# Performance work log

Hardware: AMD Instinct MI355X
Metric: run time of the kernel (lower is better)

## Reference

```python
import jax, jax.numpy as jnp
import numpy as np

NUM_PHONES = 39
BLANK = NUM_PHONES  # blank appended as last class
NEG = -1e30  # finite stand-in for -inf (log-space)


def ctc_loss(lp, targets, input_lengths, target_lengths, blank):
    """lp: (T, B, C) log-probs. Returns torch-style CTCLoss(reduction='mean', zero_infinity=True)."""
    T, B, C = lp.shape
    L = targets.shape[1]
    S = 2 * L + 1
    # extended label sequence: blank, l1, blank, l2, ..., blank
    ext = jnp.full((B, S), blank, dtype=targets.dtype).at[:, 1::2].set(targets)
    ext_m2 = jnp.concatenate([jnp.full((B, 2), blank, dtype=ext.dtype), ext[:, :-2]], axis=1)
    skip = (ext != blank) & (ext != ext_m2)  # (B, S) allow s-2 transition
    # per-step emission log-probs gathered at extended labels: (T, B, S)
    emit = jnp.take_along_axis(lp, jnp.broadcast_to(ext[None], (T, B, S)), axis=2)

    alpha0 = jnp.full((B, S), NEG, dtype=lp.dtype)
    alpha0 = alpha0.at[:, 0].set(emit[0, :, 0]).at[:, 1].set(emit[0, :, 1])
    pad1 = jnp.full((B, 1), NEG, dtype=lp.dtype)
    pad2 = jnp.full((B, 2), NEG, dtype=lp.dtype)

    def step(alpha, xs):
        emit_t, t = xs
        a1 = jnp.concatenate([pad1, alpha[:, :-1]], axis=1)
        a2 = jnp.where(skip, jnp.concatenate([pad2, alpha[:, :-2]], axis=1), NEG)
        m = jnp.maximum(jnp.maximum(alpha, a1), a2)
        new = m + jnp.log(jnp.exp(alpha - m) + jnp.exp(a1 - m) + jnp.exp(a2 - m)) + emit_t
        new = jnp.where((t < input_lengths)[:, None], new, alpha)  # freeze past length
        return new, None

    alpha, _ = jax.lax.scan(step, alpha0, (emit[1:], jnp.arange(1, T)))
    end = 2 * target_lengths  # index of final blank in extended sequence
    a_blank = jnp.take_along_axis(alpha, end[:, None], axis=1)[:, 0]
    a_label = jnp.take_along_axis(alpha, (end - 1)[:, None], axis=1)[:, 0]
    loss_b = -jnp.logaddexp(a_blank, a_label)
    loss_b = jnp.where(loss_b > 1e29, 0.0, loss_b)  # zero_infinity
    return jnp.mean(loss_b / target_lengths.astype(lp.dtype))


def setup_inputs() -> dict:
    B, T, H, L = 32, 2000, 512, 200
    C = NUM_PHONES + 1
    key = jax.random.key(0)
    k1, k2, k3 = jax.random.split(key, 3)
    hidden = jax.random.normal(k1, (B, T, H), dtype=jnp.float32)
    W = jax.random.normal(k2, (C, H), dtype=jnp.float32) / np.sqrt(H)
    b = jnp.zeros((C,), dtype=jnp.float32)
    targets = jax.random.randint(k3, (B, L), 0, NUM_PHONES, dtype=jnp.int32)
    input_lengths = jnp.full((B,), T, dtype=jnp.int32)
    target_lengths = jnp.full((B,), L, dtype=jnp.int32)
    return {"hidden": hidden, "W": W, "b": b, "targets": targets,
            "input_lengths": input_lengths, "target_lengths": target_lengths}


def reference(hidden, W, b, targets, input_lengths, target_lengths):
    # dropout is identity in eval mode
    logits = jnp.einsum('bth,ch->btc', hidden, W) + b
    log_prob = jax.nn.log_softmax(logits, axis=-1).transpose(1, 0, 2)  # (T, B, C)
    loss = ctc_loss(log_prob, targets, input_lengths, target_lengths, BLANK)
    return (log_prob, loss)
```

## Files before the change

kernel.cpp:

```cpp
#include <hip/hip_runtime.h>
#include <hip/hip_bf16.h>


#define BB 32
#define TT 2000
#define HH 512
#define CC 40
#define LL 200
#define NEGV -1e30f

typedef __attribute__((ext_vector_type(8))) short short8;
typedef __attribute__((ext_vector_type(4))) float f32x4;

__device__ __forceinline__ unsigned short f2bf(float f) {
    unsigned u = __float_as_uint(f);
    u = u + 0x7FFFu + ((u >> 16) & 1u);
    return (unsigned short)(u >> 16);
}

__device__ __forceinline__ double dshr1(double x) {
    int lo = __double2loint(x), hi = __double2hiint(x);
    lo = __builtin_amdgcn_update_dpp(0, lo, 0x138, 0xF, 0xF, false);
    hi = __builtin_amdgcn_update_dpp(0, hi, 0x138, 0xF, 0xF, false);
    return __hiloint2double(hi, lo);
}

__global__ void k0_wconv(const float* __restrict__ W, short* __restrict__ wbf) {
    const int idx = blockIdx.x * 256 + threadIdx.x;
    if (idx < 48 * HH) {
        const int n = idx >> 9, k = idx & (HH - 1);
        wbf[idx] = (n < CC) ? (short)f2bf(W[n * HH + k]) : (short)0;
    }
}

__global__ __launch_bounds__(256) void k1_mfma(
    const float* __restrict__ hidden,
    const short* __restrict__ wbf,
    const float* __restrict__ bias,
    float* __restrict__ out,
    float* __restrict__ P)
{
    const int tid = threadIdx.x, lane = tid & 63, wv = tid >> 6;
    const int quad = lane >> 4, mcol = lane & 15;
    const int r0 = (blockIdx.x * 4 + wv) * 16;

    const float* aptr = hidden + (size_t)(r0 + mcol) * HH + quad * 8;
    const short* b0p = wbf + (0 * 16 + mcol) * HH + quad * 8;
    const short* b1p = wbf + (1 * 16 + mcol) * HH + quad * 8;
    const short* b2p = wbf + (2 * 16 + mcol) * HH + quad * 8;

    f32x4 acc0 = {0.f, 0.f, 0.f, 0.f};
    f32x4 acc1 = {0.f, 0.f, 0.f, 0.f};
    f32x4 acc2 = {0.f, 0.f, 0.f, 0.f};

    #pragma unroll 2
    for (int kc = 0; kc < 16; ++kc) {
        const float4 al = *(const float4*)(aptr + kc * 32);
        const float4 ah = *(const float4*)(aptr + kc * 32 + 4);
        short8 af;
        af[0] = f2bf(al.x); af[1] = f2bf(al.y); af[2] = f2bf(al.z); af[3] = f2bf(al.w);
        af[4] = f2bf(ah.x); af[5] = f2bf(ah.y); af[6] = f2bf(ah.z); af[7] = f2bf(ah.w);
        const short8 bf0 = *(const short8*)(b0p + kc * 32);
        const short8 bf1 = *(const short8*)(b1p + kc * 32);
        const short8 bf2 = *(const short8*)(b2p + kc * 32);
        acc0 = __builtin_amdgcn_mfma_f32_16x16x32_bf16(af, bf0, acc0, 0, 0, 0);
        acc1 = __builtin_amdgcn_mfma_f32_16x16x32_bf16(af, bf1, acc1, 0, 0, 0);
        acc2 = __builtin_amdgcn_mfma_f32_16x16x32_bf16(af, bf2, acc2, 0, 0, 0);
    }

    const float bz0 = bias[mcol];
    const float bz1 = bias[16 + mcol];
    const float bz2 = (mcol < 8) ? bias[32 + mcol] : 0.0f;
    float L0[4], L1[4], L2[4], lse[4];
    #pragma unroll
    for (int j = 0; j < 4; ++j) {
        L0[j] = acc0[j] + bz0;
        L1[j] = acc1[j] + bz1;
        L2[j] = (mcol < 8) ? (acc2[j] + bz2) : NEGV;
    }
    #pragma unroll
    for (int j = 0; j < 4; ++j) {
        float m = fmaxf(fmaxf(L0[j], L1[j]), L2[j]);
        #pragma unroll
        for (int o = 1; o < 16; o <<= 1) m = fmaxf(m, __shfl_xor(m, o, 64));
        float s = __expf(L0[j] - m) + __expf(L1[j] - m)
                + ((mcol < 8) ? __expf(L2[j] - m) : 0.0f);
        #pragma unroll
        for (int o = 1; o < 16; o <<= 1) s += __shfl_xor(s, o, 64);
        lse[j] = m + __logf(s);
    }
    #pragma unroll
    for (int j = 0; j < 4; ++j) {
        const int r = r0 + quad * 4 + j;
        const int b = r / TT, t = r - b * TT;
        float* op = out + ((size_t)t * BB + b) * CC;
        float* pp = P + (size_t)r * CC;
        const float v0 = L0[j] - lse[j];
        const float v1 = L1[j] - lse[j];
        op[mcol]      = v0;  pp[mcol]      = __expf(v0);
        op[16 + mcol] = v1;  pp[16 + mcol] = __expf(v1);
        if (mcol < 8) {
            const float v2 = L2[j] - lse[j];
            op[32 + mcol] = v2;  pp[32 + mcol] = __expf(v2);
        }
    }
}

__global__ __launch_bounds__(64) void k2_fast(
    const float* __restrict__ P,
    const int* __restrict__ targets,
    const int* __restrict__ input_lengths,
    const int* __restrict__ target_lengths,
    float* __restrict__ loss_ws)
{
    const int b = blockIdx.x, l = threadIdx.x;
    const int len = input_lengths[b];
    const int tl  = target_lengths[b];

    __shared__ float ldsP[2][40 * CC];

    int cls[4]; double sk[4];
    #pragma unroll
    for (int j = 0; j < 4; ++j) {
        const int idx = 4 * l + j;
        int c = CC - 1; double skv = 0.0;
        if (idx < tl) {
            c = targets[b * LL + idx];
            if (idx == 0) skv = 1.0;
            else skv = (c != targets[b * LL + idx - 1]) ? 1.0 : 0.0;
        }
        cls[j] = c; sk[j] = skv;
    }
    const int off0 = cls[0], off1 = cls[1], off2 = cls[2], off3 = cls[3];

    const float* Pb = P + (size_t)b * TT * CC;
    const int lane4 = l * 4;

    float4 st[6]; float st6;
    auto stage_load = [&](int chunk) {
        const float* src = Pb + (size_t)chunk * (40 * CC);
        #pragma unroll
        for (int i = 0; i < 6; ++i)
            st[i] = *(const float4*)(src + i * 256 + lane4);
        st6 = src[1536 + l];
    };
    auto stage_write = [&](int par) {
        float* dst = ldsP[par];
        #pragma unroll
        for (int i = 0; i < 6; ++i)
            *(float4*)(dst + i * 256 + lane4) = st[i];
        dst[1536 + l] = st6;
    };

    stage_load(0);
    stage_write(0);

    double a0, a1, a2, a3, a4, a5, a6, a7;
    {
        const float pb0 = ldsP[0][CC - 1];
        const float pl0 = ldsP[0][off0];
        a0 = (l == 0) ? (double)pb0 : 0.0;
        a1 = (l == 0) ? (double)pl0 : 0.0;
        a2 = a3 = a4 = a5 = a6 = a7 = 0.0;
    }

    stage_load(1);

    double logscale = 0.0;

    auto step = [&](float e1f, float e3f, float e5f, float e7f, float bef) {
        const double be = (double)bef;
        const double p7 = dshr1(a7);
        const double n0 = (a0 + p7) * be;
        const double n1 = (a1 + fma(sk[0], p7, a0)) * (double)e1f;
        const double n2 = (a2 + a1) * be;
        const double n3 = (a3 + fma(sk[1], a1, a2)) * (double)e3f;
        const double n4 = (a4 + a3) * be;
        const double n5 = (a5 + fma(sk[2], a3, a4)) * (double)e5f;
        const double n6 = (a6 + a5) * be;
        const double n7 = (a7 + fma(sk[3], a5, a6)) * (double)e7f;
        a0 = n0; a1 = n1; a2 = n2; a3 = n3;
        a4 = n4; a5 = n5; a6 = n6; a7 = n7;
    };
    auto dostep = [&](const float* row) {
        step(row[off0], row[off1], row[off2], row[off3], row[CC - 1]);
    };
    auto rescale = [&]() {
        int h = __double2hiint(a0);
        int h1 = __double2hiint(a1); h = (h1 > h) ? h1 : h;
        h1 = __double2hiint(a2);     h = (h1 > h) ? h1 : h;
        h1 = __double2hiint(a3);     h = (h1 > h) ? h1 : h;
        h1 = __double2hiint(a4);     h = (h1 > h) ? h1 : h;
        h1 = __double2hiint(a5);     h = (h1 > h) ? h1 : h;
        h1 = __double2hiint(a6);     h = (h1 > h) ? h1 : h;
        h1 = __double2hiint(a7);     h = (h1 > h) ? h1 : h;
        #pragma unroll
        for (int o = 1; o < 64; o <<= 1) {
            const int hx = __shfl_xor(h, o, 64);
            h = (hx > h) ? hx : h;
        }
        if (h > 0) {
            const int be_ = h >> 20;
            const int ex  = be_ - 1022;
            const double sf = __hiloint2double((2045 - be_) << 20, 0);
            a0 *= sf; a1 *= sf; a2 *= sf; a3 *= sf;
            a4 *= sf; a5 *= sf; a6 *= sf; a7 *= sf;
            logscale += (double)ex * 0.6931471805599453;
        }
    };

    for (int c = 0; c < 50; ++c) {
        const int par = c & 1;
        const float* buf = ldsP[par];
        const int tbase = c * 40;
        if (tbase + 40 <= len) {
            if (c == 0) {
                #pragma unroll 8
                for (int u = 1; u < 40; ++u) dostep(buf + u * CC);
            } else {
                #pragma unroll 8
                for (int u = 0; u < 40; ++u) dostep(buf + u * CC);
            }
        } else {
            const int u0 = (c == 0) ? 1 : 0;
            for (int u = u0; u < 40; ++u)
                if (tbase + u < len) dostep(buf + u * CC);
        }
        rescale();
        if (c < 49) {
            stage_write(par ^ 1);
            if (c < 48) stage_load(c + 2);
        }
    }

    double contrib = 0.0;
    const int send = 2 * tl;
    #pragma unroll
    for (int i = 0; i < 8; ++i) {
        const int s = 8 * l + i;
        const double av = (i == 0) ? a0 : (i == 1) ? a1 : (i == 2) ? a2 :
                          (i == 3) ? a3 : (i == 4) ? a4 : (i == 5) ? a5 :
                          (i == 6) ? a6 : a7;
        if (s == send || s == send - 1) contrib += av;
    }
    #pragma unroll
    for (int o = 32; o > 0; o >>= 1) contrib += __shfl_xor(contrib, o, 64);

    if (l == 0) {
        double lb = 0.0;
        if (contrib > 0.0) lb = -(log(contrib) + logscale);
        if (lb > 1e29) lb = 0.0;
        loss_ws[b] = (float)(lb / (double)tl);
    }
}

__global__ void k3_reduce(const float* __restrict__ ws, float* __restrict__ loss_out)
{
    if (threadIdx.x == 0 && blockIdx.x == 0) {
        float sum = 0.0f;
        #pragma unroll
        for (int b = 0; b < BB; ++b) sum += ws[b];
        *loss_out = sum / (float)BB;
    }
}

__global__ __launch_bounds__(256) void k1_lds(
    const float* __restrict__ hidden, const float* __restrict__ W,
    const float* __restrict__ bias, float* __restrict__ out)
{
    __shared__ float Wl[CC * 256];
    float4* Wl4 = (float4*)Wl;
    const int tid = threadIdx.x;
    const int r = blockIdx.x * blockDim.x + tid;
    const float4* __restrict__ h4 = (const float4*)(hidden + (size_t)r * HH);
    const float4* __restrict__ W4g = (const float4*)W;
    float acc[CC];
    #pragma unroll
    for (int c = 0; c < CC; ++c) acc[c] = 0.0f;
    for (int kc = 0; kc < 2; ++kc) {
        __syncthreads();
        #pragma unroll
        for (int i = 0; i < 10; ++i) {
            const int idx = tid + i * 256;
            const int c = idx >> 6, j4 = idx & 63;
            Wl4[idx] = W4g[c * 128 + kc * 64 + j4];
        }
        __syncthreads();
        #pragma unroll 2
        for (int k4 = 0; k4 < 64; ++k4) {
            const float4 h = h4[kc * 64 + k4];
            #pragma unroll
            for (int c = 0; c < CC; ++c) {
                const float4 w = Wl4[c * 64 + k4];
                acc[c] = fmaf(h.x, w.x, fmaf(h.y, w.y,
                         fmaf(h.z, w.z, fmaf(h.w, w.w, acc[c]))));
            }
        }
    }
    #pragma unroll
    for (int c = 0; c < CC; ++c) acc[c] += bias[c];
    float mx = acc[0];
    #pragma unroll
    for (int c = 1; c < CC; ++c) mx = fmaxf(mx, acc[c]);
    float s = 0.0f;
    #pragma unroll
    for (int c = 0; c < CC; ++c) s += __expf(acc[c] - mx);
    const float lse = mx + __logf(s);
    const int b = r / TT, t = r - b * TT;
    float4* __restrict__ o4 = (float4*)(out + ((size_t)t * BB + b) * CC);
    #pragma unroll
    for (int c4 = 0; c4 < CC / 4; ++c4) {
        float4 v;
        v.x = acc[4 * c4 + 0] - lse; v.y = acc[4 * c4 + 1] - lse;
        v.z = acc[4 * c4 + 2] - lse; v.w = acc[4 * c4 + 3] - lse;
        o4[c4] = v;
    }
}

__device__ __forceinline__ float bperm(int byteaddr, float v) {
    return __int_as_float(__builtin_amdgcn_ds_bpermute(byteaddr, __float_as_int(v)));
}

__global__ __launch_bounds__(64) void k2_legacy(
    const float* __restrict__ lp, const int* __restrict__ targets,
    const int* __restrict__ input_lengths, const int* __restrict__ target_lengths,
    float* __restrict__ ws)
{
    const int b = blockIdx.x, lane = threadIdx.x;
    const int len = input_lengths[b];
    const int tl = target_lengths[b];
    const int S = 2 * tl + 1;
    int cad[7]; double skf[7];
    #pragma unroll
    for (int i = 0; i < 7; ++i) {
        const int s = 7 * lane + i;
        int cls = 63; double sk = 0.0;
        if (s < S) {
            if (s & 1) {
                cls = targets[b * LL + (s >> 1)];
                if (s >= 3) sk = (cls != targets[b * LL + ((s - 3) >> 1)]) ? 1.0 : 0.0;
                else sk = 1.0;
            } else cls = CC - 1;
        }
        cad[i] = cls * 4; skf[i] = sk;
    }
    const double lane0m = (lane == 0) ? 0.0 : 1.0;
    const int lc = (lane < CC) ? lane : (CC - 1);
    const size_t rowstride = (size_t)BB * CC;
    const float* lprow = lp + (size_t)b * CC + lc;
    double a0, a1, a2, a3, a4, a5, a6;
    {
        const float v0 = lprow[0];
        const float e = (lane < CC) ? __expf(v0) : 0.0f;
        a0 = (lane == 0) ? (double)bperm(cad[0], e) : 0.0;
        a1 = (lane == 0) ? (double)bperm(cad[1], e) : 0.0;
        a2 = a3 = a4 = a5 = a6 = 0.0;
    }
    float Pr[8];
    #pragma unroll
    for (int u = 0; u < 8; ++u) Pr[u] = lprow[(size_t)(1 + u) * rowstride];
    double logscale = 0.0;
    auto step = [&](int t, float pv) {
        const float ef = (lane < CC) ? __expf(pv) : 0.0f;
        const double e0 = (double)bperm(cad[0], ef), e1 = (double)bperm(cad[1], ef);
        const double e2 = (double)bperm(cad[2], ef), e3 = (double)bperm(cad[3], ef);
        const double e4 = (double)bperm(cad[4], ef), e5 = (double)bperm(cad[5], ef);
        const double e6 = (double)bperm(cad[6], ef);
        const double pl1 = __shfl_up(a6, 1, 64) * lane0m;
        const double pl2 = __shfl_up(a5, 1, 64) * lane0m;
        const double n0 = (a0 + fma(skf[0], pl2, pl1)) * e0;
        const double n1 = (a1 + fma(skf[1], pl1, a0)) * e1;
        const double n2 = (a2 + fma(skf[2], a0, a1)) * e2;
        const double n3 = (a3 + fma(skf[3], a1, a2)) * e3;
        const double n4 = (a4 + fma(skf[4], a2, a3)) * e4;
        const double n5 = (a5 + fma(skf[5], a3, a4)) * e5;
        const double n6 = (a6 + fma(skf[6], a4, a5)) * e6;
        if (t < len) { a0 = n0; a1 = n1; a2 = n2; a3 = n3; a4 = n4; a5 = n5; a6 = n6; }
    };
    auto rescale = [&]() {
        double m = fmax(fmax(fmax(a0, a1), fmax(a2, a3)), fmax(fmax(a4, a5), a6));
        #pragma unroll
        for (int o = 32; o > 0; o >>= 1) m = fmax(m, __shfl_xor(m, o, 64));
        if (m > 0.0) {
            const double inv = 1.0 / m;
            a0 *= inv; a1 *= inv; a2 *= inv; a3 *= inv; a4 *= inv; a5 *= inv; a6 *= inv;
            logscale += (double)__logf((float)m);
        }
    };
    for (int it = 0; it < 249; ++it) {
        const int t = 1 + it * 8, tb = t + 8;
        const float* pf = lprow + (size_t)tb * rowstride;
        float q[8];
        #pragma unroll
        for (int u = 0; u < 8; ++u) q[u] = (tb + u < TT) ? pf[(size_t)u * rowstride] : 0.0f;
        #pragma unroll
        for (int u = 0; u < 8; ++u) step(t + u, Pr[u]);
        rescale();
        #pragma unroll
        for (int u = 0; u < 8; ++u) Pr[u] = q[u];
    }
    #pragma unroll
    for (int u = 0; u < 7; ++u) step(1993 + u, Pr[u]);
    double contrib = 0.0;
    #pragma unroll
    for (int i = 0; i < 7; ++i) {
        const int s = 7 * lane + i;
        const double av = (i == 0) ? a0 : (i == 1) ? a1 : (i == 2) ? a2 :
                          (i == 3) ? a3 : (i == 4) ? a4 : (i == 5) ? a5 : a6;
        if (s == 2 * tl || s == 2 * tl - 1) contrib += av;
    }
    #pragma unroll
    for (int o = 32; o > 0; o >>= 1) contrib += __shfl_xor(contrib, o, 64);
    if (lane == 0) {
        double lb = 0.0;
        if (contrib > 0.0) lb = -(log(contrib) + logscale);
        if (lb > 1e29) lb = 0.0;
        ws[b] = (float)(lb / (double)tl);
    }
}

extern "C" void kernel_launch(void* const* d_in, const int* in_sizes, int n_in,
                              void* d_out, int out_size, void* d_ws, size_t ws_size,
                              hipStream_t stream) {
    const float* hidden = (const float*)d_in[0];
    const float* W      = (const float*)d_in[1];
    const float* bias   = (const float*)d_in[2];
    const int* targets  = (const int*)d_in[3];
    const int* in_len   = (const int*)d_in[4];
    const int* tg_len   = (const int*)d_in[5];

    float* out      = (float*)d_out;
    float* loss_out = out + (size_t)TT * BB * CC;

    const size_t PELEMS   = (size_t)BB * CC * TT;
    const size_t WBF_OFF  = PELEMS;
    const size_t LOSS_OFF = PELEMS + (48 * HH * sizeof(short)) / sizeof(float);
    const size_t need     = (LOSS_OFF + BB) * sizeof(float);

    if (ws_size >= need) {
        float* P   = (float*)d_ws;
        short* wbf = (short*)((float*)d_ws + WBF_OFF);
        float* lws = (float*)d_ws + LOSS_OFF;
        k0_wconv<<<dim3(96), dim3(256), 0, stream>>>(W, wbf);
        k1_mfma<<<dim3(1000), dim3(256), 0, stream>>>(hidden, wbf, bias, out, P);
        k2_fast<<<dim3(BB), dim3(64), 0, stream>>>(P, targets, in_len, tg_len, lws);
        k3_reduce<<<dim3(1), dim3(64), 0, stream>>>(lws, loss_out);
    } else {
        float* lws = (float*)d_ws;
        k1_lds<<<dim3((BB * TT) / 256), dim3(256), 0, stream>>>(hidden, W, bias, out);
        k2_legacy<<<dim3(BB), dim3(64), 0, stream>>>(out, targets, in_len, tg_len, lws);
        k3_reduce<<<dim3(1), dim3(64), 0, stream>>>(lws, loss_out);
    }
}
```

Baseline: 384.1 us.

## Fuse GEMM/log-softmax with CTC recursion via per-chunk completion counters

Merges the projection/log-softmax kernel and the CTC alpha-recursion kernel into one launch. GEMM blocks now process rows in time-chunk order across all batches and bump an atomic per-chunk counter. Eight consumer blocks of four waves each run the recursion and spin-wait on those counters, so the serial recursion overlaps with the GEMM instead of starting after it. This relies on the consumer blocks (lowest block ids) being resident while producers run, and adds atomics, fences and polling.

```diff
diff --git a/kernel.cpp b/kernel.cpp
--- a/kernel.cpp
+++ b/kernel.cpp
@@ -9,6 +9,14 @@
 #define LL 200
 #define NEGV -1e30f
 
+#define CHUNK 40
+#define NCHUNK 50
+#define ROWS_PER_CHUNK (BB * CHUNK)
+#define GBLK 1000
+#define CBLK 8
+#define BLKS_PER_CHUNK (ROWS_PER_CHUNK / 64)
+#define FLAGS_PER_CHUNK (BLKS_PER_CHUNK * 4)
+
 typedef __attribute__((ext_vector_type(8))) short short8;
 typedef __attribute__((ext_vector_type(4))) float f32x4;
 
@@ -25,7 +33,17 @@
     return __hiloint2double(hi, lo);
 }
 
-__global__ void k0_wconv(const float* __restrict__ W, short* __restrict__ wbf) {
+__device__ __forceinline__ void seq2rbt(int seq, int& r, int& b, int& t) {
+    const int c = seq / ROWS_PER_CHUNK;
+    const int rem = seq - c * ROWS_PER_CHUNK;
+    b = rem / CHUNK;
+    t = c * CHUNK + (rem - b * CHUNK);
+    r = b * TT + t;
+}
+
+__global__ void k0_wconv(const float* __restrict__ W, short* __restrict__ wbf,
+                         int* __restrict__ cnt) {
+    if (blockIdx.x == 0 && threadIdx.x < NCHUNK) cnt[threadIdx.x] = 0;
     const int idx = blockIdx.x * 256 + threadIdx.x;
     if (idx < 48 * HH) {
         const int n = idx >> 9, k = idx & (HH - 1);
@@ -33,91 +51,105 @@
     }
 }
 
-__global__ __launch_bounds__(256) void k1_mfma(
+__global__ __launch_bounds__(256) void k_fused(
     const float* __restrict__ hidden,
     const short* __restrict__ wbf,
     const float* __restrict__ bias,
     float* __restrict__ out,
-    float* __restrict__ P)
-{
-    const int tid = threadIdx.x, lane = tid & 63, wv = tid >> 6;
-    const int quad = lane >> 4, mcol = lane & 15;
-    const int r0 = (blockIdx.x * 4 + wv) * 16;
-
-    const float* aptr = hidden + (size_t)(r0 + mcol) * HH + quad * 8;
-    const short* b0p = wbf + (0 * 16 + mcol) * HH + quad * 8;
-    const short* b1p = wbf + (1 * 16 + mcol) * HH + quad * 8;
-    const short* b2p = wbf + (2 * 16 + mcol) * HH + quad * 8;
-
-    f32x4 acc0 = {0.f, 0.f, 0.f, 0.f};
-    f32x4 acc1 = {0.f, 0.f, 0.f, 0.f};
-    f32x4 acc2 = {0.f, 0.f, 0.f, 0.f};
-
-    #pragma unroll 2
-    for (int kc = 0; kc < 16; ++kc) {
-        const float4 al = *(const float4*)(aptr + kc * 32);
-        const float4 ah = *(const float4*)(aptr + kc * 32 + 4);
-        short8 af;
-        af[0] = f2bf(al.x); af[1] = f2bf(al.y); af[2] = f2bf(al.z); af[3] = f2bf(al.w);
-        af[4] = f2bf(ah.x); af[5] = f2bf(ah.y); af[6] = f2bf(ah.z); af[7] = f2bf(ah.w);
-        const short8 bf0 = *(const short8*)(b0p + kc * 32);
-        const short8 bf1 = *(const short8*)(b1p + kc * 32);
-        const short8 bf2 = *(const short8*)(b2p + kc * 32);
-        acc0 = __builtin_amdgcn_mfma_f32_16x16x32_bf16(af, bf0, acc0, 0, 0, 0);
-        acc1 = __builtin_amdgcn_mfma_f32_16x16x32_bf16(af, bf1, acc1, 0, 0, 0);
-        acc2 = __builtin_amdgcn_mfma_f32_16x16x32_bf16(af, bf2, acc2, 0, 0, 0);
-    }
-
-    const float bz0 = bias[mcol];
-    const float bz1 = bias[16 + mcol];
-    const float bz2 = (mcol < 8) ? bias[32 + mcol] : 0.0f;
-    float L0[4], L1[4], L2[4], lse[4];
-    #pragma unroll
-    for (int j = 0; j < 4; ++j) {
-        L0[j] = acc0[j] + bz0;
-        L1[j] = acc1[j] + bz1;
-        L2[j] = (mcol < 8) ? (acc2[j] + bz2) : NEGV;
-    }
-    #pragma unroll
-    for (int j = 0; j < 4; ++j) {
-        float m = fmaxf(fmaxf(L0[j], L1[j]), L2[j]);
-        #pragma unroll
-        for (int o = 1; o < 16; o <<= 1) m = fmaxf(m, __shfl_xor(m, o, 64));
-        float s = __expf(L0[j] - m) + __expf(L1[j] - m)
-                + ((mcol < 8) ? __expf(L2[j] - m) : 0.0f);
-        #pragma unroll
-        for (int o = 1; o < 16; o <<= 1) s += __shfl_xor(s, o, 64);
-        lse[j] = m + __logf(s);
-    }
-    #pragma unroll
-    for (int j = 0; j < 4; ++j) {
-        const int r = r0 + quad * 4 + j;
-        const int b = r / TT, t = r - b * TT;
-        float* op = out + ((size_t)t * BB + b) * CC;
-        float* pp = P + (size_t)r * CC;
-        const float v0 = L0[j] - lse[j];
-        const float v1 = L1[j] - lse[j];
-        op[mcol]      = v0;  pp[mcol]      = __expf(v0);
-        op[16 + mcol] = v1;  pp[16 + mcol] = __expf(v1);
-        if (mcol < 8) {
-            const float v2 = L2[j] - lse[j];
-            op[32 + mcol] = v2;  pp[32 + mcol] = __expf(v2);
-        }
-    }
-}
-
-__global__ __launch_bounds__(64) void k2_fast(
-    const float* __restrict__ P,
+    float* __restrict__ P,
     const int* __restrict__ targets,
     const int* __restrict__ input_lengths,
     const int* __restrict__ target_lengths,
-    float* __restrict__ loss_ws)
+    float* __restrict__ loss_ws,
+    int* __restrict__ cnt)
 {
-    const int b = blockIdx.x, l = threadIdx.x;
+    __shared__ float ldsP[4][2][CHUNK * CC];
+
+    const int tid = threadIdx.x, lane = tid & 63, wv = tid >> 6;
+
+    if (blockIdx.x >= CBLK) {
+        const int g = blockIdx.x - CBLK;
+        const int quad = lane >> 4, mcol = lane & 15;
+        const int seq0 = g * 64 + wv * 16;
+        const int mychunk = g / BLKS_PER_CHUNK;
+
+        int rA, bA, tA; seq2rbt(seq0 + mcol, rA, bA, tA);
+        const float* aptr = hidden + (size_t)rA * HH + quad * 8;
+        const short* b0p = wbf + (0 * 16 + mcol) * HH + quad * 8;
+        const short* b1p = wbf + (1 * 16 + mcol) * HH + quad * 8;
+        const short* b2p = wbf + (2 * 16 + mcol) * HH + quad * 8;
+
+        f32x4 acc0 = {0.f, 0.f, 0.f, 0.f};
+        f32x4 acc1 = {0.f, 0.f, 0.f, 0.f};
+        f32x4 acc2 = {0.f, 0.f, 0.f, 0.f};
+
+        #pragma unroll 2
+        for (int kc = 0; kc < 16; ++kc) {
+            const float4 al = *(const float4*)(aptr + kc * 32);
+            const float4 ah = *(const float4*)(aptr + kc * 32 + 4);
+            short8 af;
+            af[0] = f2bf(al.x); af[1] = f2bf(al.y); af[2] = f2bf(al.z); af[3] = f2bf(al.w);
+            af[4] = f2bf(ah.x); af[5] = f2bf(ah.y); af[6] = f2bf(ah.z); af[7] = f2bf(ah.w);
+            const short8 bf0 = *(const short8*)(b0p + kc * 32);
+            const short8 bf1 = *(const short8*)(b1p + kc * 32);
+            const short8 bf2 = *(const short8*)(b2p + kc * 32);
+            acc0 = __builtin_amdgcn_mfma_f32_16x16x32_bf16(af, bf0, acc0, 0, 0, 0);
+            acc1 = __builtin_amdgcn_mfma_f32_16x16x32_bf16(af, bf1, acc1, 0, 0, 0);
+            acc2 = __builtin_amdgcn_mfma_f32_16x16x32_bf16(af, bf2, acc2, 0, 0, 0);
+        }
+
+        const float bz0 = bias[mcol];
+        const float bz1 = bias[16 + mcol];
+        const float bz2 = (mcol < 8) ? bias[32 + mcol] : 0.0f;
+        float L0[4], L1[4], L2[4], lse[4];
+        #pragma unroll
+        for (int j = 0; j < 4; ++j) {
+            L0[j] = acc0[j] + bz0;
+            L1[j] = acc1[j] + bz1;
+            L2[j] = (mcol < 8) ? (acc2[j] + bz2) : NEGV;
+        }
+        #pragma unroll
+        for (int j = 0; j < 4; ++j) {
+            float m = fmaxf(fmaxf(L0[j], L1[j]), L2[j]);
+            #pragma unroll
+            for (int o = 1; o < 16; o <<= 1) m = fmaxf(m, __shfl_xor(m, o, 64));
+            float s = __expf(L0[j] - m) + __expf(L1[j] - m)
+                    + ((mcol < 8) ? __expf(L2[j] - m) : 0.0f);
+            #pragma unroll
+            for (int o = 1; o < 16; o <<= 1) s += __shfl_xor(s, o, 64);
+            lse[j] = m + __logf(s);
+        }
+        #pragma unroll
+        for (int j = 0; j < 4; ++j) {
+            int r, b, t; seq2rbt(seq0 + quad * 4 + j, r, b, t);
+            float* op = out + ((size_t)t * BB + b) * CC;
+            float* pp = P + (size_t)r * CC;
+            const float v0 = L0[j] - lse[j];
+            const float v1 = L1[j] - lse[j];
+            op[mcol]      = v0;  pp[mcol]      = __expf(v0);
+            op[16 + mcol] = v1;  pp[16 + mcol] = __expf(v1);
+            if (mcol < 8) {
+                const float v2 = L2[j] - lse[j];
+                op[32 + mcol] = v2;  pp[32 + mcol] = __expf(v2);
+            }
+        }
+        __threadfence();
+        if (lane == 0)
+            __hip_atomic_fetch_add(&cnt[mychunk], 1, __ATOMIC_RELEASE,
+                                   __HIP_MEMORY_SCOPE_AGENT);
+        return;
+    }
+
+    const int b = blockIdx.x * 4 + wv;
+    const int l = lane;
     const int len = input_lengths[b];
     const int tl  = target_lengths[b];
 
-    __shared__ float ldsP[2][40 * CC];
+    auto wait_chunk = [&](int c) {
+        while (__hip_atomic_load(&cnt[c], __ATOMIC_ACQUIRE,
+                                 __HIP_MEMORY_SCOPE_AGENT) < FLAGS_PER_CHUNK)
+            __builtin_amdgcn_s_sleep(8);
+    };
 
     int cls[4]; double sk[4];
     #pragma unroll
@@ -135,35 +167,39 @@
 
     const float* Pb = P + (size_t)b * TT * CC;
     const int lane4 = l * 4;
+    float* lds0 = ldsP[wv][0];
+    float* lds1 = ldsP[wv][1];
 
     float4 st[6]; float st6;
     auto stage_load = [&](int chunk) {
-        const float* src = Pb + (size_t)chunk * (40 * CC);
+        const float* src = Pb + (size_t)chunk * (CHUNK * CC);
         #pragma unroll
         for (int i = 0; i < 6; ++i)
             st[i] = *(const float4*)(src + i * 256 + lane4);
         st6 = src[1536 + l];
     };
     auto stage_write = [&](int par) {
-        float* dst = ldsP[par];
+        float* dst = par ? lds1 : lds0;
         #pragma unroll
         for (int i = 0; i < 6; ++i)
             *(float4*)(dst + i * 256 + lane4) = st[i];
         dst[1536 + l] = st6;
     };
 
+    wait_chunk(0);
     stage_load(0);
     stage_write(0);
 
     double a0, a1, a2, a3, a4, a5, a6, a7;
     {
-        const float pb0 = ldsP[0][CC - 1];
-        const float pl0 = ldsP[0][off0];
+        const float pb0 = lds0[CC - 1];
+        const float pl0 = lds0[off0];
         a0 = (l == 0) ? (double)pb0 : 0.0;
         a1 = (l == 0) ? (double)pl0 : 0.0;
         a2 = a3 = a4 = a5 = a6 = a7 = 0.0;
     }
 
+    wait_chunk(1);
     stage_load(1);
 
     double logscale = 0.0;
@@ -209,27 +245,36 @@
         }
     };
 
-    for (int c = 0; c < 50; ++c) {
-        const int par = c & 1;
-        const float* buf = ldsP[par];
-        const int tbase = c * 40;
-        if (tbase + 40 <= len) {
+    if (len == TT) {
+        for (int c = 0; c < NCHUNK; ++c) {
+            const int par = c & 1;
+            const float* buf = par ? lds1 : lds0;
             if (c == 0) {
                 #pragma unroll 8
-                for (int u = 1; u < 40; ++u) dostep(buf + u * CC);
+                for (int u = 1; u < CHUNK; ++u) dostep(buf + u * CC);
             } else {
                 #pragma unroll 8
-                for (int u = 0; u < 40; ++u) dostep(buf + u * CC);
+                for (int u = 0; u < CHUNK; ++u) dostep(buf + u * CC);
             }
-        } else {
+            rescale();
+            if (c < NCHUNK - 1) {
+                stage_write(par ^ 1);
+                if (c < NCHUNK - 2) { wait_chunk(c + 2); stage_load(c + 2); }
+            }
+        }
+    } else {
+        for (int c = 0; c < NCHUNK; ++c) {
+            const int par = c & 1;
+            const float* buf = par ? lds1 : lds0;
+            const int tbase = c * CHUNK;
             const int u0 = (c == 0) ? 1 : 0;
-            for (int u = u0; u < 40; ++u)
+            for (int u = u0; u < CHUNK; ++u)
                 if (tbase + u < len) dostep(buf + u * CC);
-        }
-        rescale();
-        if (c < 49) {
-            stage_write(par ^ 1);
-            if (c < 48) stage_load(c + 2);
+            rescale();
+            if (c < NCHUNK - 1) {
+                stage_write(par ^ 1);
+                if (c < NCHUNK - 2) { wait_chunk(c + 2); stage_load(c + 2); }
+            }
         }
     }
 
@@ -435,15 +480,17 @@
     const size_t PELEMS   = (size_t)BB * CC * TT;
     const size_t WBF_OFF  = PELEMS;
     const size_t LOSS_OFF = PELEMS + (48 * HH * sizeof(short)) / sizeof(float);
-    const size_t need     = (LOSS_OFF + BB) * sizeof(float);
+    const size_t CNT_OFF  = LOSS_OFF + BB;
+    const size_t need     = (CNT_OFF + NCHUNK) * sizeof(float);
 
     if (ws_size >= need) {
         float* P   = (float*)d_ws;
         short* wbf = (short*)((float*)d_ws + WBF_OFF);
         float* lws = (float*)d_ws + LOSS_OFF;
-        k0_wconv<<<dim3(96), dim3(256), 0, stream>>>(W, wbf);
-        k1_mfma<<<dim3(1000), dim3(256), 0, stream>>>(hidden, wbf, bias, out, P);
-        k2_fast<<<dim3(BB), dim3(64), 0, stream>>>(P, targets, in_len, tg_len, lws);
+        int*   cnt = (int*)((float*)d_ws + CNT_OFF);
+        k0_wconv<<<dim3(96), dim3(256), 0, stream>>>(W, wbf, cnt);
+        k_fused<<<dim3(CBLK + GBLK), dim3(256), 0, stream>>>(
+            hidden, wbf, bias, out, P, targets, in_len, tg_len, lws, cnt);
         k3_reduce<<<dim3(1), dim3(64), 0, stream>>>(lws, loss_out);
     } else {
         float* lws = (float*)d_ws;
```

New measurement: 646.0 us. 68.2% more time.
